# Optimization experiments

Measured on AMD Instinct MI355X. Metric: run time of the kernel, lower is better.

Reference implementation:

```python
import jax, jax.numpy as jnp
import numpy as np

B, T, H = 512, 256, 256


def setup_inputs() -> dict:
    key = jax.random.key(0)
    ks = jax.random.split(key, 12)
    s = 1.0 / np.sqrt(H)
    return {
        "h_tilde": jax.random.normal(ks[0], (B, H), jnp.float32),
        "c_t": jax.random.normal(ks[1], (B, H), jnp.float32),
        "h_history": jax.random.normal(ks[2], (B, T, H), jnp.float32),
        "deltaT_hist": jax.random.uniform(ks[3], (B, T, 1), jnp.float32),
        "deltaL_hist": jax.random.uniform(ks[4], (B, T, 1), jnp.float32),
        "W_I": jax.random.normal(ks[5], (H, 2 * H), jnp.float32) * s,
        "W_Ih": jax.random.normal(ks[6], (H, H), jnp.float32) * s,
        "W_I1T": jax.random.normal(ks[7], (H, 1), jnp.float32),
        "W_I1L": jax.random.normal(ks[8], (H, 1), jnp.float32),
        "b_I": jnp.zeros((H,), jnp.float32),
        "W_oI": jax.random.normal(ks[9], (H, H), jnp.float32) * s,
        "b_oI": jnp.zeros((H,), jnp.float32),
        "v_t": jax.random.normal(ks[10], (H,), jnp.float32),
    }


def reference(h_tilde, c_t, h_history, deltaT_hist, deltaL_hist,
              W_I, W_Ih, W_I1T, W_I1L, b_I, W_oI, b_oI, v_t):
    # h_hat: [B, 2H]; current projection: [B, H]
    h_hat = jnp.concatenate([h_tilde, c_t], axis=1)
    current_proj = h_hat @ W_I.T
    # Batched per-step additive attention pre-activation I_ti: [B, T, H]
    I = (current_proj[:, None, :]
         + jnp.einsum('bth,oh->bto', h_history, W_Ih)
         + deltaT_hist * W_I1T[:, 0]          # [B,T,1]*[H] -> [B,T,H]
         + deltaL_hist * W_I1L[:, 0]
         + b_I)
    o = jnp.tanh(jnp.einsum('bti,oi->bto', I, W_oI) + b_oI)  # [B, T, H]
    scores = jnp.einsum('bth,h->bt', o, v_t)                  # [B, T]
    alpha = jax.nn.softmax(scores, axis=1)
    s_t = jnp.einsum('bt,bth->bh', alpha, h_history)          # [B, H]
    return (s_t, alpha)
```

## Files before the change

kernel.cpp:

```cpp
#include <hip/hip_runtime.h>
#include <hip/hip_bf16.h>
#include <hip/hip_fp16.h>

#define Hdim 256
#define Tdim 256
#define Bdim 512
#define TT   64
#define NTILE (Tdim / TT)
#define NTHR 256
#define NCP  32

typedef __attribute__((ext_vector_type(8))) short s16x8;
typedef __attribute__((ext_vector_type(8))) _Float16 f16x8;
typedef __attribute__((ext_vector_type(2))) _Float16 f16x2;
typedef __attribute__((ext_vector_type(4))) float f32x4;
typedef unsigned short u16;
typedef unsigned int u32;

__device__ __forceinline__ u32 cvt_pk_f16(float lo, float hi) {
    auto v = __builtin_amdgcn_cvt_pkrtz(lo, hi);
    return __builtin_bit_cast(u32, v);
}
__device__ __forceinline__ u16 f2h_rne(float x) {
    _Float16 h = (_Float16)x;
    return __builtin_bit_cast(u16, h);
}
__device__ __forceinline__ f32x4 mfma16h(s16x8 a, s16x8 b, f32x4 c) {
    return __builtin_amdgcn_mfma_f32_16x16x32_f16(
        __builtin_bit_cast(f16x8, a), __builtin_bit_cast(f16x8, b), c, 0, 0, 0);
}
__device__ __forceinline__ float fast_tanh(float z) {
    float e = __expf(2.0f * z);
    return 1.0f - 2.0f * __builtin_amdgcn_rcpf(e + 1.0f);
}
__device__ __forceinline__ s16x8 bfrag_f32(const float* __restrict__ wp) {
    float4 x0 = *(const float4*)(wp + 0);
    float4 x1 = *(const float4*)(wp + 4);
    uint4 uu = make_uint4(cvt_pk_f16(x0.x, x0.y), cvt_pk_f16(x0.z, x0.w),
                          cvt_pk_f16(x1.x, x1.y), cvt_pk_f16(x1.z, x1.w));
    return __builtin_bit_cast(s16x8, uu);
}

__global__ __launch_bounds__(256) void prep_kernel(
        const float* __restrict__ W_Ih, const float* __restrict__ W_oI,
        const float* __restrict__ W_I1T, const float* __restrict__ W_I1L,
        const float* __restrict__ h_tilde, const float* __restrict__ c_t,
        const float* __restrict__ W_I, const float* __restrict__ b_I,
        const float* __restrict__ b_oI,
        u16* __restrict__ Wph, float* __restrict__ wT2, float* __restrict__ wL2,
        float* __restrict__ cp2) {
    __shared__ char smem[24576];
    __shared__ float redT[4], redL[4];
    const int tid = threadIdx.x;
    const int w = tid >> 6, lane = tid & 63;
    const int c = lane & 15, g = lane >> 4;

    if (blockIdx.x < Hdim) {
        float* sWo = (float*)smem;
        const int o = blockIdx.x;
        const int j = tid;
        sWo[j] = W_oI[o * Hdim + j];
        __syncthreads();
        float a0 = 0.f, a1 = 0.f, a2 = 0.f, a3 = 0.f;
        #pragma unroll 8
        for (int i = 0; i < Hdim; i += 4) {
            a0 += sWo[i + 0] * W_Ih[(i + 0) * Hdim + j];
            a1 += sWo[i + 1] * W_Ih[(i + 1) * Hdim + j];
            a2 += sWo[i + 2] * W_Ih[(i + 2) * Hdim + j];
            a3 += sWo[i + 3] * W_Ih[(i + 3) * Hdim + j];
        }
        const float acc = (a0 + a1) + (a2 + a3);
        const int dst = (o >> 4) * 4096 + (j >> 5) * 512 + ((j >> 3) & 3) * 128
                      + (o & 15) * 8 + (j & 7);
        Wph[dst] = f2h_rne(acc);
        float pT = sWo[j] * W_I1T[j];
        float pL = sWo[j] * W_I1L[j];
        #pragma unroll
        for (int d = 1; d < 64; d <<= 1) {
            pT += __shfl_xor(pT, d, 64);
            pL += __shfl_xor(pL, d, 64);
        }
        if (lane == 0) { redT[w] = pT; redL[w] = pL; }
        __syncthreads();
        if (j == 0) {
            wT2[o] = redT[0] + redT[1] + redT[2] + redT[3];
            wL2[o] = redL[0] + redL[1] + redL[2] + redL[3];
        }
    } else {
        char* hh_b  = smem;
        char* cpl_b = smem + 16384;
        const int b0 = (blockIdx.x - Hdim) * 16;
        const u32 swzA = (u32)((c & 7) << 4);
        const f32x4 fz = {0.f, 0.f, 0.f, 0.f};

        {
            const int srow = tid >> 4;
            const int sj = tid & 15;
            const u32 sbb = (u32)(srow * 1024);
            const u32 ssz = (u32)((srow & 7) << 4);
            #pragma unroll
            for (int ch = 0; ch < 2; ++ch) {
                const int col = sj * 32 + ch * 16;
                const float* src = (col < Hdim)
                    ? (h_tilde + (size_t)(b0 + srow) * Hdim + col)
                    : (c_t + (size_t)(b0 + srow) * Hdim + col - Hdim);
                float4 f0 = *(const float4*)(src + 0);
                float4 f1 = *(const float4*)(src + 4);
                float4 f2 = *(const float4*)(src + 8);
                float4 f3 = *(const float4*)(src + 12);
                uint4 ua = make_uint4(cvt_pk_f16(f0.x, f0.y), cvt_pk_f16(f0.z, f0.w),
                                      cvt_pk_f16(f1.x, f1.y), cvt_pk_f16(f1.z, f1.w));
                uint4 ub = make_uint4(cvt_pk_f16(f2.x, f2.y), cvt_pk_f16(f2.z, f2.w),
                                      cvt_pk_f16(f3.x, f3.y), cvt_pk_f16(f3.z, f3.w));
                *(uint4*)(hh_b + ((sbb + (u32)(col * 2) + 0) ^ ssz)) = ua;
                *(uint4*)(hh_b + ((sbb + (u32)(col * 2) + 16) ^ ssz)) = ub;
            }
        }
        __syncthreads();

        f32x4 acc[4];
        #pragma unroll
        for (int n = 0; n < 4; ++n) acc[n] = fz;
        #pragma unroll
        for (int ks = 0; ks < 16; ++ks) {
            const s16x8 a = *(const s16x8*)(hh_b +
                (((u32)(c * 1024 + ks * 64 + g * 16)) ^ swzA));
            #pragma unroll
            for (int n = 0; n < 4; ++n) {
                const int o = w * 64 + n * 16 + c;
                const s16x8 bf = bfrag_f32(W_I + (size_t)o * (2 * Hdim) + ks * 32 + g * 8);
                acc[n] = mfma16h(a, bf, acc[n]);
            }
        }
        #pragma unroll
        for (int n = 0; n < 4; ++n) {
            const int o = w * 64 + n * 16 + c;
            const float bi = b_I[o];
            const u32 ocol2 = (u32)((o & ~1) * 2);
            #pragma unroll
            for (int r = 0; r < 4; ++r) {
                const int row = g * 4 + r;
                float z = acc[n][r] + bi;
                float zsw = __shfl_xor(z, 1, 64);
                if (!(c & 1)) {
                    u32 h2 = cvt_pk_f16(z, zsw);
                    *(u32*)(cpl_b + (((u32)(row * 512) + ocol2) ^ ((u32)((row & 7) << 4)))) = h2;
                }
            }
        }
        __syncthreads();

        f32x4 acc2[4];
        #pragma unroll
        for (int n = 0; n < 4; ++n) acc2[n] = fz;
        #pragma unroll
        for (int ks = 0; ks < 8; ++ks) {
            const s16x8 a = *(const s16x8*)(cpl_b +
                (((u32)(c * 512 + ks * 64 + g * 16)) ^ swzA));
            #pragma unroll
            for (int n = 0; n < 4; ++n) {
                const int o = w * 64 + n * 16 + c;
                const s16x8 bf = bfrag_f32(W_oI + (size_t)o * Hdim + ks * 32 + g * 8);
                acc2[n] = mfma16h(a, bf, acc2[n]);
            }
        }
        #pragma unroll
        for (int n = 0; n < 4; ++n) {
            const int o = w * 64 + n * 16 + c;
            const float bo = b_oI[o];
            #pragma unroll
            for (int r = 0; r < 4; ++r)
                cp2[(size_t)(b0 + g * 4 + r) * Hdim + o] = acc2[n][r] + bo;
        }
    }
}

__global__ __launch_bounds__(NTHR, 4) void scores_kernel(
        const float* __restrict__ hist, const float* __restrict__ dT,
        const float* __restrict__ dL, const float* __restrict__ cp2,
        const u16* __restrict__ Wph,
        const float* __restrict__ wT2, const float* __restrict__ wL2,
        const float* __restrict__ v_t, float* __restrict__ scores,
        float* __restrict__ Spart, float* __restrict__ mpart,
        float* __restrict__ lpart) {
    __shared__ u16 lds_u[TT * Hdim];
    __shared__ float dtl[TT], dll[TT];
    __shared__ float sc_part[4][TT];
    __shared__ float p_sh[TT];
    __shared__ float ml_sh[2];
    __shared__ float sacc2[2][Hdim];

    const int bid = blockIdx.x;
    const int b = bid >> 2;
    const int t0 = (bid & 3) * TT;
    const int tid = threadIdx.x;
    const int w = tid >> 6, lane = tid & 63;
    const int c = lane & 15, g = lane >> 4;
    const int ob = w * 64;

    const int wfrag = lane * 8;
    #define WOFF(n, ks) ((w * 4 + (n)) * 4096 + (ks) * 512 + wfrag)

    if (tid < TT) {
        dtl[tid] = dT[b * Tdim + t0 + tid];
        dll[tid] = dL[b * Tdim + t0 + tid];
    }

    {
        const int srow = tid >> 2;
        const int sj = tid & 3;
        const float* srcb = hist + ((size_t)b * Tdim + t0 + srow) * Hdim;
        const u32 sbb = (u32)(srow * 512);
        const u32 ssz = (u32)((srow & 7) << 4);
        char* dst = (char*)lds_u;
        #pragma unroll
        for (int ch = 0; ch < 4; ++ch) {
            const int col = ch * 64 + sj * 16;
            float4 f0 = *(const float4*)(srcb + col + 0);
            float4 f1 = *(const float4*)(srcb + col + 4);
            float4 f2 = *(const float4*)(srcb + col + 8);
            float4 f3 = *(const float4*)(srcb + col + 12);
            uint4 ua = make_uint4(cvt_pk_f16(f0.x, f0.y), cvt_pk_f16(f0.z, f0.w),
                                  cvt_pk_f16(f1.x, f1.y), cvt_pk_f16(f1.z, f1.w));
            uint4 ub = make_uint4(cvt_pk_f16(f2.x, f2.y), cvt_pk_f16(f2.z, f2.w),
                                  cvt_pk_f16(f3.x, f3.y), cvt_pk_f16(f3.z, f3.w));
            *(uint4*)(dst + ((sbb + (u32)(col * 2) + 0) ^ ssz)) = ua;
            *(uint4*)(dst + ((sbb + (u32)(col * 2) + 16) ^ ssz)) = ub;
        }
    }
    __syncthreads();

    const f32x4 fz = {0.f, 0.f, 0.f, 0.f};
    const u32 swzA = (u32)((c & 7) << 4);

    f32x4 acc[4][4];
    #pragma unroll
    for (int m = 0; m < 4; ++m)
        #pragma unroll
        for (int n = 0; n < 4; ++n) acc[m][n] = fz;
    {
        const char* hb = (const char*)lds_u;
        #pragma unroll
        for (int ks = 0; ks < 8; ++ks) {
            s16x8 a[4];
            #pragma unroll
            for (int m = 0; m < 4; ++m)
                a[m] = *(const s16x8*)(hb +
                    (((u32)((m * 16 + c) * 512 + g * 16 + ks * 64)) ^ swzA));
            #pragma unroll
            for (int n = 0; n < 4; ++n) {
                const s16x8 bh = *(const s16x8*)(Wph + WOFF(n, ks));
                #pragma unroll
                for (int m = 0; m < 4; ++m)
                    acc[m][n] = mfma16h(a[m], bh, acc[m][n]);
            }
        }
    }

    float cpv[4], wtv[4], wlv[4], vvv[4];
    #pragma unroll
    for (int n = 0; n < 4; ++n) {
        const int o = ob + n * 16 + c;
        cpv[n] = cp2[(size_t)b * Hdim + o];
        wtv[n] = wT2[o];
        wlv[n] = wL2[o];
        vvv[n] = v_t[o];
    }
    #pragma unroll
    for (int m = 0; m < 4; ++m) {
        #pragma unroll
        for (int r = 0; r < 4; ++r) {
            const int row = m * 16 + g * 4 + r;
            const float dtr = dtl[row], dlr = dll[row];
            float s = 0.f;
            #pragma unroll
            for (int n = 0; n < 4; ++n) {
                float z = acc[m][n][r] + cpv[n] + dtr * wtv[n] + dlr * wlv[n];
                s += fast_tanh(z) * vvv[n];
            }
            s += __shfl_xor(s, 1, 64);
            s += __shfl_xor(s, 2, 64);
            s += __shfl_xor(s, 4, 64);
            s += __shfl_xor(s, 8, 64);
            if (c == 0) sc_part[w][row] = s;
        }
    }
    __syncthreads();

    if (tid < TT) {
        float s = sc_part[0][tid] + sc_part[1][tid] + sc_part[2][tid] + sc_part[3][tid];
        scores[b * Tdim + t0 + tid] = s;
        float mx = s;
        #pragma unroll
        for (int d = 1; d < 64; d <<= 1) mx = fmaxf(mx, __shfl_xor(mx, d, 64));
        float p = __expf(s - mx);
        float l = p;
        #pragma unroll
        for (int d = 1; d < 64; d <<= 1) l += __shfl_xor(l, d, 64);
        p_sh[tid] = p;
        if (tid == 0) { ml_sh[0] = mx; ml_sh[1] = l; }
    }
    __syncthreads();

    {
        const int half = tid >> 7;
        const int pp = tid & 127;
        const char* hb = (const char*)lds_u;
        float s0 = 0.f, s1 = 0.f;
        #pragma unroll 8
        for (int i = 0; i < 32; ++i) {
            const int t = half * 32 + i;
            const float pv = p_sh[t];
            const u32 hw = *(const u32*)(hb + (((u32)(t * 512 + pp * 4)) ^ ((u32)((t & 7) << 4))));
            const f16x2 hv = __builtin_bit_cast(f16x2, hw);
            s0 += pv * (float)hv[0];
            s1 += pv * (float)hv[1];
        }
        sacc2[half][2 * pp] = s0;
        sacc2[half][2 * pp + 1] = s1;
    }
    __syncthreads();
    Spart[(size_t)bid * Hdim + tid] = sacc2[0][tid] + sacc2[1][tid];
    if (tid == 0) { mpart[bid] = ml_sh[0]; lpart[bid] = ml_sh[1]; }
    #undef WOFF
}

__global__ __launch_bounds__(256) void combine_kernel(
        const float* __restrict__ Spart, const float* __restrict__ mpart,
        const float* __restrict__ lpart, float* __restrict__ out) {
    const int b = blockIdx.x;
    const int tid = threadIdx.x;
    __shared__ float fsh[4], inv_l_sh, m_sh;
    if (tid == 0) {
        const float m0 = mpart[4 * b + 0], m1 = mpart[4 * b + 1];
        const float m2 = mpart[4 * b + 2], m3 = mpart[4 * b + 3];
        const float m = fmaxf(fmaxf(m0, m1), fmaxf(m2, m3));
        const float f0 = __expf(m0 - m), f1 = __expf(m1 - m);
        const float f2 = __expf(m2 - m), f3 = __expf(m3 - m);
        const float l = f0 * lpart[4 * b + 0] + f1 * lpart[4 * b + 1]
                      + f2 * lpart[4 * b + 2] + f3 * lpart[4 * b + 3];
        fsh[0] = f0; fsh[1] = f1; fsh[2] = f2; fsh[3] = f3;
        inv_l_sh = 1.0f / l;
        m_sh = m;
    }
    __syncthreads();
    const float inv_l = inv_l_sh;
    const float S = fsh[0] * Spart[(size_t)(4 * b + 0) * Hdim + tid]
                  + fsh[1] * Spart[(size_t)(4 * b + 1) * Hdim + tid]
                  + fsh[2] * Spart[(size_t)(4 * b + 2) * Hdim + tid]
                  + fsh[3] * Spart[(size_t)(4 * b + 3) * Hdim + tid];
    out[b * Hdim + tid] = S * inv_l;
    float* scores = out + Bdim * Hdim;
    const float sc = scores[b * Tdim + tid];
    scores[b * Tdim + tid] = __expf(sc - m_sh) * inv_l;
}

extern "C" void kernel_launch(void* const* d_in, const int* in_sizes, int n_in,
                              void* d_out, int out_size, void* d_ws, size_t ws_size,
                              hipStream_t stream) {
    const float* h_tilde = (const float*)d_in[0];
    const float* c_t     = (const float*)d_in[1];
    const float* hist    = (const float*)d_in[2];
    const float* dT      = (const float*)d_in[3];
    const float* dL      = (const float*)d_in[4];
    const float* W_I     = (const float*)d_in[5];
    const float* W_Ih    = (const float*)d_in[6];
    const float* W_I1T   = (const float*)d_in[7];
    const float* W_I1L   = (const float*)d_in[8];
    const float* b_I     = (const float*)d_in[9];
    const float* W_oI    = (const float*)d_in[10];
    const float* b_oI    = (const float*)d_in[11];
    const float* v_t     = (const float*)d_in[12];
    float* out = (float*)d_out;

    char* ws = (char*)d_ws;
    u16* Wph     = (u16*)ws;
    float* cp2   = (float*)(ws + 131072);
    float* wT2   = (float*)(ws + 655360);
    float* wL2   = (float*)(ws + 656384);
    float* Spart = (float*)(ws + 657408);
    float* mpart = (float*)(ws + 657408 + 2097152);
    float* lpart = (float*)(ws + 657408 + 2105344);
    float* scores = out + Bdim * Hdim;

    prep_kernel<<<dim3(Hdim + NCP), dim3(256), 0, stream>>>(
        W_Ih, W_oI, W_I1T, W_I1L, h_tilde, c_t, W_I, b_I, b_oI,
        Wph, wT2, wL2, cp2);
    scores_kernel<<<dim3(Bdim * NTILE), dim3(NTHR), 0, stream>>>(
        hist, dT, dL, cp2, Wph, wT2, wL2, v_t, scores, Spart, mpart, lpart);
    combine_kernel<<<dim3(Bdim), dim3(256), 0, stream>>>(Spart, mpart, lpart, out);
}
```

Baseline: 80.59 us.

## Stage history tile as fp32 in LDS via direct global-to-LDS loads

The scores kernel now copies the h_history tile straight into shared memory in fp32 with global_load_lds, using a swizzled layout. It no longer goes through registers and fp16 conversion during staging. The conversion to fp16 moves into the MFMA A-fragment reads, and the weighted-sum stage reads fp32 directly. LDS use doubles to 64KB per block and the launch-bounds occupancy hint of 4 is dropped. This lowers how many blocks fit per CU in exchange for a cheaper, asynchronous load path.

```diff
diff --git a/kernel.cpp b/kernel.cpp
--- a/kernel.cpp
+++ b/kernel.cpp
@@ -39,6 +39,11 @@
     uint4 uu = make_uint4(cvt_pk_f16(x0.x, x0.y), cvt_pk_f16(x0.z, x0.w),
                           cvt_pk_f16(x1.x, x1.y), cvt_pk_f16(x1.z, x1.w));
     return __builtin_bit_cast(s16x8, uu);
+}
+__device__ __forceinline__ void gload_lds16(const void* g, void* l) {
+    __builtin_amdgcn_global_load_lds(
+        (const __attribute__((address_space(1))) unsigned int*)g,
+        (__attribute__((address_space(3))) unsigned int*)l, 16, 0, 0);
 }
 
 __global__ __launch_bounds__(256) void prep_kernel(
@@ -92,7 +97,6 @@
         const int b0 = (blockIdx.x - Hdim) * 16;
         const u32 swzA = (u32)((c & 7) << 4);
         const f32x4 fz = {0.f, 0.f, 0.f, 0.f};
-
         {
             const int srow = tid >> 4;
             const int sj = tid & 15;
@@ -117,7 +121,6 @@
             }
         }
         __syncthreads();
-
         f32x4 acc[4];
         #pragma unroll
         for (int n = 0; n < 4; ++n) acc[n] = fz;
@@ -149,7 +152,6 @@
             }
         }
         __syncthreads();
-
         f32x4 acc2[4];
         #pragma unroll
         for (int n = 0; n < 4; ++n) acc2[n] = fz;
@@ -175,7 +177,7 @@
     }
 }
 
-__global__ __launch_bounds__(NTHR, 4) void scores_kernel(
+__global__ __launch_bounds__(NTHR) void scores_kernel(
         const float* __restrict__ hist, const float* __restrict__ dT,
         const float* __restrict__ dL, const float* __restrict__ cp2,
         const u16* __restrict__ Wph,
@@ -183,7 +185,7 @@
         const float* __restrict__ v_t, float* __restrict__ scores,
         float* __restrict__ Spart, float* __restrict__ mpart,
         float* __restrict__ lpart) {
-    __shared__ u16 lds_u[TT * Hdim];
+    __shared__ float lds_f[TT * Hdim];
     __shared__ float dtl[TT], dll[TT];
     __shared__ float sc_part[4][TT];
     __shared__ float p_sh[TT];
@@ -201,37 +203,26 @@
     const int wfrag = lane * 8;
     #define WOFF(n, ks) ((w * 4 + (n)) * 4096 + (ks) * 512 + wfrag)
 
+    {
+        const float* hrow = hist + ((size_t)b * Tdim + t0 + w * 16) * Hdim;
+        char* lrow = (char*)lds_f + (w * 16) * 1024;
+        const int goff = (int)((((lane >> 1) ^ 0) << 3) | ((lane & 1) << 2));
+        #pragma unroll
+        for (int i = 0; i < 16; ++i) {
+            const int row7 = (w * 16 + i) & 7;
+            const int gl = ((lane >> 1) ^ row7);
+            gload_lds16(hrow + (size_t)i * Hdim + gl * 8 + (lane & 1) * 4,
+                        lrow + i * 1024);
+        }
+        (void)goff;
+    }
     if (tid < TT) {
         dtl[tid] = dT[b * Tdim + t0 + tid];
         dll[tid] = dL[b * Tdim + t0 + tid];
     }
-
-    {
-        const int srow = tid >> 2;
-        const int sj = tid & 3;
-        const float* srcb = hist + ((size_t)b * Tdim + t0 + srow) * Hdim;
-        const u32 sbb = (u32)(srow * 512);
-        const u32 ssz = (u32)((srow & 7) << 4);
-        char* dst = (char*)lds_u;
-        #pragma unroll
-        for (int ch = 0; ch < 4; ++ch) {
-            const int col = ch * 64 + sj * 16;
-            float4 f0 = *(const float4*)(srcb + col + 0);
-            float4 f1 = *(const float4*)(srcb + col + 4);
-            float4 f2 = *(const float4*)(srcb + col + 8);
-            float4 f3 = *(const float4*)(srcb + col + 12);
-            uint4 ua = make_uint4(cvt_pk_f16(f0.x, f0.y), cvt_pk_f16(f0.z, f0.w),
-                                  cvt_pk_f16(f1.x, f1.y), cvt_pk_f16(f1.z, f1.w));
-            uint4 ub = make_uint4(cvt_pk_f16(f2.x, f2.y), cvt_pk_f16(f2.z, f2.w),
-                                  cvt_pk_f16(f3.x, f3.y), cvt_pk_f16(f3.z, f3.w));
-            *(uint4*)(dst + ((sbb + (u32)(col * 2) + 0) ^ ssz)) = ua;
-            *(uint4*)(dst + ((sbb + (u32)(col * 2) + 16) ^ ssz)) = ub;
-        }
-    }
     __syncthreads();
 
     const f32x4 fz = {0.f, 0.f, 0.f, 0.f};
-    const u32 swzA = (u32)((c & 7) << 4);
 
     f32x4 acc[4][4];
     #pragma unroll
@@ -239,14 +230,20 @@
         #pragma unroll
         for (int n = 0; n < 4; ++n) acc[m][n] = fz;
     {
-        const char* hb = (const char*)lds_u;
+        const char* hb = (const char*)lds_f;
         #pragma unroll
         for (int ks = 0; ks < 8; ++ks) {
             s16x8 a[4];
             #pragma unroll
-            for (int m = 0; m < 4; ++m)
-                a[m] = *(const s16x8*)(hb +
-                    (((u32)((m * 16 + c) * 512 + g * 16 + ks * 64)) ^ swzA));
+            for (int m = 0; m < 4; ++m) {
+                const u32 ad = (u32)((m * 16 + c) * 1024
+                             + ((u32)((ks * 4 + g) ^ (c & 7)) << 5));
+                float4 x0 = *(const float4*)(hb + ad);
+                float4 x1 = *(const float4*)(hb + ad + 16);
+                uint4 uu = make_uint4(cvt_pk_f16(x0.x, x0.y), cvt_pk_f16(x0.z, x0.w),
+                                      cvt_pk_f16(x1.x, x1.y), cvt_pk_f16(x1.z, x1.w));
+                a[m] = __builtin_bit_cast(s16x8, uu);
+            }
             #pragma unroll
             for (int n = 0; n < 4; ++n) {
                 const s16x8 bh = *(const s16x8*)(Wph + WOFF(n, ks));
@@ -305,16 +302,17 @@
     {
         const int half = tid >> 7;
         const int pp = tid & 127;
-        const char* hb = (const char*)lds_u;
+        const char* hb = (const char*)lds_f;
         float s0 = 0.f, s1 = 0.f;
         #pragma unroll 8
         for (int i = 0; i < 32; ++i) {
             const int t = half * 32 + i;
             const float pv = p_sh[t];
-            const u32 hw = *(const u32*)(hb + (((u32)(t * 512 + pp * 4)) ^ ((u32)((t & 7) << 4))));
-            const f16x2 hv = __builtin_bit_cast(f16x2, hw);
-            s0 += pv * (float)hv[0];
-            s1 += pv * (float)hv[1];
+            const u32 ad = (u32)(t * 1024
+                         + (((u32)((pp >> 2) ^ (t & 7)) << 5) | (u32)((pp & 3) * 8)));
+            const float2 hv = *(const float2*)(hb + ad);
+            s0 += pv * hv.x;
+            s1 += pv * hv.y;
         }
         sacc2[half][2 * pp] = s0;
         sacc2[half][2 * pp + 1] = s1;
```

New measurement: 89.70 us. 1.11x slower.
